# Optimization experiments

Measured on AMD Instinct MI355X. Metric: run time of the kernel, lower is better.

The kernel has to match this reference:

```python
import jax, jax.numpy as jnp
import numpy as np

# Static config (matches init_kwargs)
THR = 0.2
BORDER = 2
TEMP = 0.1
H0C, W0C = 60, 80
H1C, W1C = 60, 80
HW0_I = (480, 640)
SCALE = HW0_I[0] / H0C  # = 8.0, coarse->image scale


def setup_inputs() -> dict:
    key = jax.random.key(0)
    k0, k1 = jax.random.split(key)
    feat0 = jax.random.normal(k0, (4, H0C * W0C, 256), dtype=jnp.float32)
    feat1 = jax.random.normal(k1, (4, H1C * W1C, 256), dtype=jnp.float32)
    return {"feat0": feat0, "feat1": feat1}


def _valid_axis(n):
    i = jnp.arange(n)
    return (i >= BORDER) & (i < n - BORDER)


def reference(feat0, feat1):
    B, L, C = feat0.shape
    S = feat1.shape[1]
    inv_sqrt_c = 1.0 / jnp.sqrt(jnp.asarray(C, feat0.dtype))
    f0 = feat0 * inv_sqrt_c
    f1 = feat1 * inv_sqrt_c
    # similarity + dual softmax -> confidence matrix [B, L, S]
    sim = jnp.einsum("blc,bsc->bls", f0, f1) / TEMP
    conf = jax.nn.softmax(sim, axis=1) * jax.nn.softmax(sim, axis=2)

    # threshold + border removal (static border, no padding masks)
    mask = conf > THR
    m5 = mask.reshape(B, H0C, W0C, H1C, W1C)
    m5 = (m5
          & _valid_axis(H0C)[None, :, None, None, None]
          & _valid_axis(W0C)[None, None, :, None, None]
          & _valid_axis(H1C)[None, None, None, :, None]
          & _valid_axis(W1C)[None, None, None, None, :])
    mask = m5.reshape(B, L, S)

    # mutual nearest: keep conf only where it is both the row max and the col max
    score = mask.astype(conf.dtype) * jnp.max(conf, axis=2, keepdims=True) * jnp.max(conf, axis=1, keepdims=True)
    mask_max_values = jnp.max(score, axis=2)          # [B, L]
    s_ids = jnp.argmax(score, axis=2)                 # [B, L]
    match = mask_max_values > 0                       # [B, L] dense stand-in for torch.where
    mconf = jnp.take_along_axis(conf, s_ids[:, :, None], axis=2)[..., 0]
    mconf = jnp.where(match, mconf, jnp.zeros_like(mconf))

    # coarse keypoint coordinates
    l = jnp.arange(L)
    mkpts0 = jnp.stack([l % W0C, l // W0C], axis=1).astype(conf.dtype) * SCALE          # [L, 2]
    mkpts1 = jnp.stack([s_ids % W1C, s_ids // W1C], axis=-1).astype(conf.dtype) * SCALE  # [B, L, 2]
    return conf, match, s_ids, mconf, mkpts0, mkpts1
```

## Files before the change

kernel.cpp:

```cpp
#include <hip/hip_runtime.h>
#include <math.h>

#define B_ 4
#define L_ 4800
#define S_ 4800
#define C_ 256
#define LP_ 4864
#define THR 0.2f
#define SIM_SCALE 0.0390625f
#define KPT_SCALE 8.0f
#define CAND_CAP 262144u

typedef short bf16x8 __attribute__((ext_vector_type(8)));
typedef float f32x4  __attribute__((ext_vector_type(4)));

#define WS_ZERO_N 115204
#define WS_CAND_CNT 115200
#define WS_CAND_LIST 115208
#define WS_BF16 (115208 + CAND_CAP)

__device__ __forceinline__ unsigned short f2bf(float x) {
    union { float f; unsigned int u; } v; v.f = x;
    unsigned int r = v.u + 0x7fffu + ((v.u >> 16) & 1u);
    return (unsigned short)(r >> 16);
}

__device__ __forceinline__ void gload_lds16(const ushort* g, ushort* l) {
    __builtin_amdgcn_global_load_lds(
        (const __attribute__((address_space(1))) unsigned int*)g,
        (__attribute__((address_space(3))) unsigned int*)l,
        16, 0, 0);
}

__global__ void k_cast(const float* __restrict__ f0, const float* __restrict__ f1,
                       ushort* __restrict__ f0b, ushort* __restrict__ f1b,
                       float* __restrict__ ws) {
    const int i = blockIdx.x * blockDim.x + threadIdx.x;
    if (i < WS_ZERO_N) ws[i] = 0.0f;
    if (i * 4 >= B_ * L_ * C_) return;
    const int perb = L_ * C_ / 4;
    const int b    = i / perb;
    const int rem  = i - b * perb;
    float4 a = ((const float4*)f0)[i];
    float4 v = ((const float4*)f1)[i];
    ushort4 oa, ob;
    oa.x = f2bf(a.x); oa.y = f2bf(a.y); oa.z = f2bf(a.z); oa.w = f2bf(a.w);
    ob.x = f2bf(v.x); ob.y = f2bf(v.y); ob.z = f2bf(v.z); ob.w = f2bf(v.w);
    const int o = b * (LP_ * C_ / 4) + rem;
    ((ushort4*)f0b)[o] = oa;
    ((ushort4*)f1b)[o] = ob;
}

template <int PASS>
__global__ __launch_bounds__(256) void k_gemm(
        const ushort* __restrict__ f0b, const ushort* __restrict__ f1b,
        float* __restrict__ conf,
        float* __restrict__ rowsum, float* __restrict__ colsum,
        float* __restrict__ rowmax, float* __restrict__ colmax,
        unsigned* __restrict__ cand_cnt, unsigned* __restrict__ cand_list) {
    const int b    = blockIdx.z;
    const int l0   = blockIdx.y * 128;
    const int n0   = blockIdx.x * 128;
    const int t    = threadIdx.x;
    const int lane = t & 63;
    const int wid  = t >> 6;
    const int quad = lane >> 4;
    const int lr   = lane & 15;
    const int wr   = wid >> 1, wc = wid & 1;
    const int lw0  = l0 + wr * 64;
    const int nw0  = n0 + wc * 64;

    __shared__ ushort lA[128 * 32];
    __shared__ ushort lB[128 * 32];

    const ushort* A  = f0b + (size_t)b * LP_ * C_;
    const ushort* Bm = f1b + (size_t)b * LP_ * C_;

    f32x4 acc[4][4];
#pragma unroll
    for (int r = 0; r < 4; r++)
#pragma unroll
        for (int c = 0; c < 4; c++) acc[r][c] = (f32x4){0.f, 0.f, 0.f, 0.f};

    for (int kk = 0; kk < C_; kk += 32) {
#pragma unroll
        for (int i = 0; i < 2; i++) {
            const int e   = i * 256 + t;
            const int row = e >> 2;
            const int ch  = e & 3;
            gload_lds16(A  + (size_t)(l0 + row) * C_ + kk + ch * 8, &lA[e * 8]);
            gload_lds16(Bm + (size_t)(n0 + row) * C_ + kk + ch * 8, &lB[e * 8]);
        }
        __syncthreads();
        bf16x8 af[4], bf[4];
#pragma unroll
        for (int r = 0; r < 4; r++)
            af[r] = *(const bf16x8*)&lA[(wr * 64 + r * 16 + lr) * 32 + quad * 8];
#pragma unroll
        for (int c = 0; c < 4; c++)
            bf[c] = *(const bf16x8*)&lB[(wc * 64 + c * 16 + lr) * 32 + quad * 8];
#pragma unroll
        for (int r = 0; r < 4; r++)
#pragma unroll
            for (int c = 0; c < 4; c++)
                acc[r][c] = __builtin_amdgcn_mfma_f32_16x16x32_bf16(af[r], bf[c], acc[r][c], 0, 0, 0);
        __syncthreads();
    }

#pragma unroll
    for (int r = 0; r < 4; r++)
#pragma unroll
        for (int c = 0; c < 4; c++)
#pragma unroll
            for (int g = 0; g < 4; g++)
                acc[r][c][g] = __expf(acc[r][c][g] * SIM_SCALE);

    const bool edge = (lw0 + 63 >= L_) || (nw0 + 63 >= S_);
    if (edge) {
#pragma unroll
        for (int r = 0; r < 4; r++)
#pragma unroll
            for (int c = 0; c < 4; c++)
#pragma unroll
                for (int g = 0; g < 4; g++) {
                    const int l = lw0 + r * 16 + quad * 4 + g;
                    const int s = nw0 + c * 16 + lr;
                    if (l >= L_ || s >= S_) acc[r][c][g] = 0.f;
                }
    }

    if constexpr (PASS == 0) {
#pragma unroll
        for (int r = 0; r < 4; r++)
#pragma unroll
            for (int g = 0; g < 4; g++) {
                float v = acc[r][0][g] + acc[r][1][g] + acc[r][2][g] + acc[r][3][g];
                v += __shfl_xor(v, 1, 64);
                v += __shfl_xor(v, 2, 64);
                v += __shfl_xor(v, 4, 64);
                v += __shfl_xor(v, 8, 64);
                const int row = lw0 + r * 16 + quad * 4 + g;
                if (lr == 0 && row < L_) atomicAdd(rowsum + b * L_ + row, v);
            }
#pragma unroll
        for (int c = 0; c < 4; c++) {
            float v = 0.f;
#pragma unroll
            for (int r = 0; r < 4; r++)
#pragma unroll
                for (int g = 0; g < 4; g++) v += acc[r][c][g];
            v += __shfl_xor(v, 16, 64);
            v += __shfl_xor(v, 32, 64);
            const int s = nw0 + c * 16 + lr;
            if (quad == 0 && s < S_) atomicAdd(colsum + b * S_ + s, v);
        }
    } else {
        float irs[4][4];
#pragma unroll
        for (int r = 0; r < 4; r++)
#pragma unroll
            for (int g = 0; g < 4; g++) {
                const int l = lw0 + r * 16 + quad * 4 + g;
                irs[r][g] = 1.0f / rowsum[b * L_ + (l < L_ ? l : L_ - 1)];
            }
        float ics[4];
#pragma unroll
        for (int c = 0; c < 4; c++) {
            const int s = nw0 + c * 16 + lr;
            ics[c] = 1.0f / colsum[b * S_ + (s < S_ ? s : S_ - 1)];
        }
#pragma unroll
        for (int r = 0; r < 4; r++)
#pragma unroll
            for (int c = 0; c < 4; c++)
#pragma unroll
                for (int g = 0; g < 4; g++) {
                    const float p = acc[r][c][g];
                    acc[r][c][g] = p * p * (irs[r][g] * ics[c]);
                }

        float* pb = conf + (size_t)b * L_ * S_;
        if (!edge) {
#pragma unroll
            for (int r = 0; r < 4; r++)
#pragma unroll
                for (int g = 0; g < 4; g++) {
                    const int row = lw0 + r * 16 + quad * 4 + g;
                    float* prow = pb + (size_t)row * S_ + nw0 + lr;
#pragma unroll
                    for (int c = 0; c < 4; c++) prow[c * 16] = acc[r][c][g];
                }
        } else {
#pragma unroll
            for (int r = 0; r < 4; r++)
#pragma unroll
                for (int g = 0; g < 4; g++) {
                    const int row = lw0 + r * 16 + quad * 4 + g;
                    if (row < L_) {
                        float* prow = pb + (size_t)row * S_ + nw0 + lr;
#pragma unroll
                        for (int c = 0; c < 4; c++)
                            if (nw0 + c * 16 + lr < S_) prow[c * 16] = acc[r][c][g];
                    }
                }
        }

        float lane_max = 0.f;
#pragma unroll
        for (int r = 0; r < 4; r++)
#pragma unroll
            for (int g = 0; g < 4; g++) {
                float m = fmaxf(fmaxf(acc[r][0][g], acc[r][1][g]),
                                fmaxf(acc[r][2][g], acc[r][3][g]));
                lane_max = fmaxf(lane_max, m);
                m = fmaxf(m, __shfl_xor(m, 1, 64));
                m = fmaxf(m, __shfl_xor(m, 2, 64));
                m = fmaxf(m, __shfl_xor(m, 4, 64));
                m = fmaxf(m, __shfl_xor(m, 8, 64));
                const int row = lw0 + r * 16 + quad * 4 + g;
                if (lr == 0 && row < L_)
                    atomicMax((unsigned*)rowmax + b * L_ + row, __float_as_uint(m));
            }
#pragma unroll
        for (int c = 0; c < 4; c++) {
            float v = 0.f;
#pragma unroll
            for (int r = 0; r < 4; r++)
#pragma unroll
                for (int g = 0; g < 4; g++) v = fmaxf(v, acc[r][c][g]);
            v = fmaxf(v, __shfl_xor(v, 16, 64));
            v = fmaxf(v, __shfl_xor(v, 32, 64));
            const int s = nw0 + c * 16 + lr;
            if (quad == 0 && s < S_)
                atomicMax((unsigned*)colmax + b * S_ + s, __float_as_uint(v));
        }

        if (__any(lane_max > THR)) {
#pragma unroll
            for (int r = 0; r < 4; r++)
#pragma unroll
                for (int c = 0; c < 4; c++)
#pragma unroll
                    for (int g = 0; g < 4; g++) {
                        const float v = acc[r][c][g];
                        if (v > THR) {
                            const int l = lw0 + r * 16 + quad * 4 + g;
                            const int s = nw0 + c * 16 + lr;
                            const int lh = l / 80, lw = l % 80;
                            const int sh = s / 80, sw = s % 80;
                            if (lh >= 2 && lh < 58 && lw >= 2 && lw < 78 &&
                                sh >= 2 && sh < 58 && sw >= 2 && sw < 78) {
                                unsigned idx = atomicAdd(cand_cnt, 1u);
                                if (idx < CAND_CAP)
                                    cand_list[idx] = ((unsigned)b << 26) |
                                                     ((unsigned)l << 13) | (unsigned)s;
                            }
                        }
                    }
        }
    }
}

__global__ void k_score(const unsigned* __restrict__ cand_cnt,
                        const unsigned* __restrict__ cand_list,
                        const float* __restrict__ rowmax,
                        const float* __restrict__ colmax,
                        unsigned long long* __restrict__ best) {
    const unsigned n = min(*cand_cnt, CAND_CAP);
    for (unsigned i = blockIdx.x * blockDim.x + threadIdx.x; i < n;
         i += gridDim.x * blockDim.x) {
        const unsigned pk = cand_list[i];
        const int b = pk >> 26;
        const int l = (pk >> 13) & 8191;
        const int s = pk & 8191;
        const float sc = rowmax[b * L_ + l] * colmax[b * S_ + s];
        const unsigned long long key =
            ((unsigned long long)__float_as_uint(sc) << 32) |
            (unsigned long long)(0xFFFFFFFFu - (unsigned)s);
        atomicMax(best + b * L_ + l, key);
    }
}

__global__ void k_emit(const float* __restrict__ conf,
                       const unsigned long long* __restrict__ best,
                       float* __restrict__ o_match, float* __restrict__ o_sids,
                       float* __restrict__ o_mconf, float* __restrict__ o_kp0,
                       float* __restrict__ o_kp1) {
    const int i = blockIdx.x * blockDim.x + threadIdx.x;
    if (i >= B_ * L_) return;
    const int b = i / L_;
    const int l = i - b * L_;
    const unsigned long long key = best[i];
    const bool match = key != 0ull;
    const int sid = match ? (int)(0xFFFFFFFFu - (unsigned)(key & 0xFFFFFFFFull)) : 0;
    const float mc = match ? conf[(size_t)i * S_ + sid] : 0.0f;
    o_match[i] = match ? 1.0f : 0.0f;
    o_sids[i]  = (float)sid;
    o_mconf[i] = mc;
    o_kp1[i * 2 + 0] = (float)(sid % 80) * KPT_SCALE;
    o_kp1[i * 2 + 1] = (float)(sid / 80) * KPT_SCALE;
    if (b == 0) {
        o_kp0[l * 2 + 0] = (float)(l % 80) * KPT_SCALE;
        o_kp0[l * 2 + 1] = (float)(l / 80) * KPT_SCALE;
    }
}

extern "C" void kernel_launch(void* const* d_in, const int* in_sizes, int n_in,
                              void* d_out, int out_size, void* d_ws, size_t ws_size,
                              hipStream_t stream) {
    const float* f0 = (const float*)d_in[0];
    const float* f1 = (const float*)d_in[1];
    float* out = (float*)d_out;

    float* conf_o  = out;
    float* o_match = out + (size_t)92160000;
    float* o_sids  = o_match + 19200;
    float* o_mconf = o_sids + 19200;
    float* o_kp0   = o_mconf + 19200;
    float* o_kp1   = o_kp0 + 9600;

    float* wsf    = (float*)d_ws;
    float* rowsum = wsf;
    float* colsum = wsf + 19200;
    float* rowmax = wsf + 38400;
    float* colmax = wsf + 57600;
    unsigned long long* best = (unsigned long long*)(wsf + 76800);
    unsigned* cand_cnt  = (unsigned*)(wsf + WS_CAND_CNT);
    unsigned* cand_list = (unsigned*)(wsf + WS_CAND_LIST);
    ushort* f0b = (ushort*)(wsf + WS_BF16);
    ushort* f1b = f0b + (size_t)B_ * LP_ * C_;

    k_cast<<<4800, 256, 0, stream>>>(f0, f1, f0b, f1b, wsf);
    k_gemm<0><<<dim3(38, 38, B_), 256, 0, stream>>>(
        f0b, f1b, conf_o, rowsum, colsum, rowmax, colmax, cand_cnt, cand_list);
    k_gemm<1><<<dim3(38, 38, B_), 256, 0, stream>>>(
        f0b, f1b, conf_o, rowsum, colsum, rowmax, colmax, cand_cnt, cand_list);
    k_score<<<64, 256, 0, stream>>>(cand_cnt, cand_list, rowmax, colmax, best);
    k_emit<<<75, 256, 0, stream>>>(conf_o, best, o_match, o_sids, o_mconf, o_kp0, o_kp1);
}
```

Before: 646.0 us.

## Replace second GEMM pass with streaming normalization kernel over stored exp values

The GEMM now runs once, writing exp(sim) into the conf buffer while accumulating row and column sums. A new bandwidth-bound kernel rereads conf, applies the dual-softmax normalisation, writes it back, and computes row/col maxima plus threshold candidates using shared-memory reductions. This removes the recomputation of the full similarity GEMM. In exchange it adds an extra full read and write of the large conf tensor.

```diff
diff --git a/kernel.cpp b/kernel.cpp
--- a/kernel.cpp
+++ b/kernel.cpp
@@ -51,13 +51,10 @@
     ((ushort4*)f1b)[o] = ob;
 }
 
-template <int PASS>
 __global__ __launch_bounds__(256) void k_gemm(
         const ushort* __restrict__ f0b, const ushort* __restrict__ f1b,
         float* __restrict__ conf,
-        float* __restrict__ rowsum, float* __restrict__ colsum,
-        float* __restrict__ rowmax, float* __restrict__ colmax,
-        unsigned* __restrict__ cand_cnt, unsigned* __restrict__ cand_list) {
+        float* __restrict__ rowsum, float* __restrict__ colsum) {
     const int b    = blockIdx.z;
     const int l0   = blockIdx.y * 128;
     const int n0   = blockIdx.x * 128;
@@ -129,135 +126,121 @@
                 }
     }
 
-    if constexpr (PASS == 0) {
+    float* pb = conf + (size_t)b * L_ * S_;
+    if (!edge) {
 #pragma unroll
         for (int r = 0; r < 4; r++)
 #pragma unroll
             for (int g = 0; g < 4; g++) {
-                float v = acc[r][0][g] + acc[r][1][g] + acc[r][2][g] + acc[r][3][g];
-                v += __shfl_xor(v, 1, 64);
-                v += __shfl_xor(v, 2, 64);
-                v += __shfl_xor(v, 4, 64);
-                v += __shfl_xor(v, 8, 64);
                 const int row = lw0 + r * 16 + quad * 4 + g;
-                if (lr == 0 && row < L_) atomicAdd(rowsum + b * L_ + row, v);
+                float* prow = pb + (size_t)row * S_ + nw0 + lr;
+#pragma unroll
+                for (int c = 0; c < 4; c++) prow[c * 16] = acc[r][c][g];
             }
-#pragma unroll
-        for (int c = 0; c < 4; c++) {
-            float v = 0.f;
-#pragma unroll
-            for (int r = 0; r < 4; r++)
-#pragma unroll
-                for (int g = 0; g < 4; g++) v += acc[r][c][g];
-            v += __shfl_xor(v, 16, 64);
-            v += __shfl_xor(v, 32, 64);
-            const int s = nw0 + c * 16 + lr;
-            if (quad == 0 && s < S_) atomicAdd(colsum + b * S_ + s, v);
+    } else {
+#pragma unroll
+        for (int r = 0; r < 4; r++)
+#pragma unroll
+            for (int g = 0; g < 4; g++) {
+                const int row = lw0 + r * 16 + quad * 4 + g;
+                if (row < L_) {
+                    float* prow = pb + (size_t)row * S_ + nw0 + lr;
+#pragma unroll
+                    for (int c = 0; c < 4; c++)
+                        if (nw0 + c * 16 + lr < S_) prow[c * 16] = acc[r][c][g];
+                }
+            }
+    }
+
+#pragma unroll
+    for (int r = 0; r < 4; r++)
+#pragma unroll
+        for (int g = 0; g < 4; g++) {
+            float v = acc[r][0][g] + acc[r][1][g] + acc[r][2][g] + acc[r][3][g];
+            v += __shfl_xor(v, 1, 64);
+            v += __shfl_xor(v, 2, 64);
+            v += __shfl_xor(v, 4, 64);
+            v += __shfl_xor(v, 8, 64);
+            const int row = lw0 + r * 16 + quad * 4 + g;
+            if (lr == 0 && row < L_) atomicAdd(rowsum + b * L_ + row, v);
         }
-    } else {
-        float irs[4][4];
-#pragma unroll
-        for (int r = 0; r < 4; r++)
-#pragma unroll
-            for (int g = 0; g < 4; g++) {
-                const int l = lw0 + r * 16 + quad * 4 + g;
-                irs[r][g] = 1.0f / rowsum[b * L_ + (l < L_ ? l : L_ - 1)];
-            }
-        float ics[4];
-#pragma unroll
-        for (int c = 0; c < 4; c++) {
-            const int s = nw0 + c * 16 + lr;
-            ics[c] = 1.0f / colsum[b * S_ + (s < S_ ? s : S_ - 1)];
-        }
-#pragma unroll
-        for (int r = 0; r < 4; r++)
-#pragma unroll
-            for (int c = 0; c < 4; c++)
-#pragma unroll
-                for (int g = 0; g < 4; g++) {
-                    const float p = acc[r][c][g];
-                    acc[r][c][g] = p * p * (irs[r][g] * ics[c]);
-                }
-
-        float* pb = conf + (size_t)b * L_ * S_;
-        if (!edge) {
-#pragma unroll
-            for (int r = 0; r < 4; r++)
-#pragma unroll
-                for (int g = 0; g < 4; g++) {
-                    const int row = lw0 + r * 16 + quad * 4 + g;
-                    float* prow = pb + (size_t)row * S_ + nw0 + lr;
-#pragma unroll
-                    for (int c = 0; c < 4; c++) prow[c * 16] = acc[r][c][g];
-                }
-        } else {
-#pragma unroll
-            for (int r = 0; r < 4; r++)
-#pragma unroll
-                for (int g = 0; g < 4; g++) {
-                    const int row = lw0 + r * 16 + quad * 4 + g;
-                    if (row < L_) {
-                        float* prow = pb + (size_t)row * S_ + nw0 + lr;
-#pragma unroll
-                        for (int c = 0; c < 4; c++)
-                            if (nw0 + c * 16 + lr < S_) prow[c * 16] = acc[r][c][g];
+#pragma unroll
+    for (int c = 0; c < 4; c++) {
+        float v = 0.f;
+#pragma unroll
+        for (int r = 0; r < 4; r++)
+#pragma unroll
+            for (int g = 0; g < 4; g++) v += acc[r][c][g];
+        v += __shfl_xor(v, 16, 64);
+        v += __shfl_xor(v, 32, 64);
+        const int s = nw0 + c * 16 + lr;
+        if (quad == 0 && s < S_) atomicAdd(colsum + b * S_ + s, v);
+    }
+}
+
+__global__ __launch_bounds__(256) void k_norm(
+        float* __restrict__ conf,
+        const float* __restrict__ rowsum, const float* __restrict__ colsum,
+        float* __restrict__ rowmax, float* __restrict__ colmax,
+        unsigned* __restrict__ cand_cnt, unsigned* __restrict__ cand_list) {
+    const int b  = blockIdx.z;
+    const int l0 = blockIdx.y * 64;
+    const int s0 = blockIdx.x * 64;
+    __shared__ unsigned rm[64], cm[64];
+    const int t = threadIdx.x;
+    if (t < 64) { rm[t] = 0u; cm[t] = 0u; }
+    __syncthreads();
+    const int c4 = t & 15, r0 = t >> 4;
+    const int sbase = s0 + c4 * 4;
+    const float4 cs = *(const float4*)(colsum + b * S_ + sbase);
+    const float icx = 1.0f / cs.x, icy = 1.0f / cs.y, icz = 1.0f / cs.z, icw = 1.0f / cs.w;
+    float cmx = 0.f, cmy = 0.f, cmz = 0.f, cmw = 0.f;
+    float* base = conf + (size_t)b * L_ * S_;
+#pragma unroll
+    for (int it = 0; it < 4; it++) {
+        const int r = r0 + 16 * it;
+        const int l = l0 + r;
+        const float irs = 1.0f / rowsum[b * L_ + l];
+        float* addr = base + (size_t)l * S_ + sbase;
+        float4 p = *(float4*)addr;
+        float4 cf;
+        cf.x = p.x * p.x * (irs * icx);
+        cf.y = p.y * p.y * (irs * icy);
+        cf.z = p.z * p.z * (irs * icz);
+        cf.w = p.w * p.w * (irs * icw);
+        *(float4*)addr = cf;
+        const float m = fmaxf(fmaxf(cf.x, cf.y), fmaxf(cf.z, cf.w));
+        atomicMax(&rm[r], __float_as_uint(m));
+        cmx = fmaxf(cmx, cf.x); cmy = fmaxf(cmy, cf.y);
+        cmz = fmaxf(cmz, cf.z); cmw = fmaxf(cmw, cf.w);
+        if (m > THR) {
+            const int lh = l / 80, lw = l % 80;
+            if (lh >= 2 && lh < 58 && lw >= 2 && lw < 78) {
+                const float cfa[4] = {cf.x, cf.y, cf.z, cf.w};
+#pragma unroll
+                for (int j = 0; j < 4; j++) {
+                    if (cfa[j] > THR) {
+                        const int s = sbase + j;
+                        const int sh = s / 80, sw = s % 80;
+                        if (sh >= 2 && sh < 58 && sw >= 2 && sw < 78) {
+                            unsigned idx = atomicAdd(cand_cnt, 1u);
+                            if (idx < CAND_CAP)
+                                cand_list[idx] = ((unsigned)b << 26) |
+                                                 ((unsigned)l << 13) | (unsigned)s;
+                        }
                     }
                 }
+            }
         }
-
-        float lane_max = 0.f;
-#pragma unroll
-        for (int r = 0; r < 4; r++)
-#pragma unroll
-            for (int g = 0; g < 4; g++) {
-                float m = fmaxf(fmaxf(acc[r][0][g], acc[r][1][g]),
-                                fmaxf(acc[r][2][g], acc[r][3][g]));
-                lane_max = fmaxf(lane_max, m);
-                m = fmaxf(m, __shfl_xor(m, 1, 64));
-                m = fmaxf(m, __shfl_xor(m, 2, 64));
-                m = fmaxf(m, __shfl_xor(m, 4, 64));
-                m = fmaxf(m, __shfl_xor(m, 8, 64));
-                const int row = lw0 + r * 16 + quad * 4 + g;
-                if (lr == 0 && row < L_)
-                    atomicMax((unsigned*)rowmax + b * L_ + row, __float_as_uint(m));
-            }
-#pragma unroll
-        for (int c = 0; c < 4; c++) {
-            float v = 0.f;
-#pragma unroll
-            for (int r = 0; r < 4; r++)
-#pragma unroll
-                for (int g = 0; g < 4; g++) v = fmaxf(v, acc[r][c][g]);
-            v = fmaxf(v, __shfl_xor(v, 16, 64));
-            v = fmaxf(v, __shfl_xor(v, 32, 64));
-            const int s = nw0 + c * 16 + lr;
-            if (quad == 0 && s < S_)
-                atomicMax((unsigned*)colmax + b * S_ + s, __float_as_uint(v));
-        }
-
-        if (__any(lane_max > THR)) {
-#pragma unroll
-            for (int r = 0; r < 4; r++)
-#pragma unroll
-                for (int c = 0; c < 4; c++)
-#pragma unroll
-                    for (int g = 0; g < 4; g++) {
-                        const float v = acc[r][c][g];
-                        if (v > THR) {
-                            const int l = lw0 + r * 16 + quad * 4 + g;
-                            const int s = nw0 + c * 16 + lr;
-                            const int lh = l / 80, lw = l % 80;
-                            const int sh = s / 80, sw = s % 80;
-                            if (lh >= 2 && lh < 58 && lw >= 2 && lw < 78 &&
-                                sh >= 2 && sh < 58 && sw >= 2 && sw < 78) {
-                                unsigned idx = atomicAdd(cand_cnt, 1u);
-                                if (idx < CAND_CAP)
-                                    cand_list[idx] = ((unsigned)b << 26) |
-                                                     ((unsigned)l << 13) | (unsigned)s;
-                            }
-                        }
-                    }
-        }
+    }
+    atomicMax(&cm[c4 * 4 + 0], __float_as_uint(cmx));
+    atomicMax(&cm[c4 * 4 + 1], __float_as_uint(cmy));
+    atomicMax(&cm[c4 * 4 + 2], __float_as_uint(cmz));
+    atomicMax(&cm[c4 * 4 + 3], __float_as_uint(cmw));
+    __syncthreads();
+    if (t < 64) {
+        atomicMax((unsigned*)rowmax + b * L_ + l0 + t, rm[t]);
+        atomicMax((unsigned*)colmax + b * S_ + s0 + t, cm[t]);
     }
 }
 
@@ -331,10 +314,9 @@
     ushort* f1b = f0b + (size_t)B_ * LP_ * C_;
 
     k_cast<<<4800, 256, 0, stream>>>(f0, f1, f0b, f1b, wsf);
-    k_gemm<0><<<dim3(38, 38, B_), 256, 0, stream>>>(
-        f0b, f1b, conf_o, rowsum, colsum, rowmax, colmax, cand_cnt, cand_list);
-    k_gemm<1><<<dim3(38, 38, B_), 256, 0, stream>>>(
-        f0b, f1b, conf_o, rowsum, colsum, rowmax, colmax, cand_cnt, cand_list);
+    k_gemm<<<dim3(38, 38, B_), 256, 0, stream>>>(f0b, f1b, conf_o, rowsum, colsum);
+    k_norm<<<dim3(75, 75, B_), 256, 0, stream>>>(conf_o, rowsum, colsum,
+                                                 rowmax, colmax, cand_cnt, cand_list);
     k_score<<<64, 256, 0, stream>>>(cand_cnt, cand_list, rowmax, colmax, best);
     k_emit<<<75, 256, 0, stream>>>(conf_o, best, o_match, o_sids, o_mconf, o_kp0, o_kp1);
 }
```

Result: faster. 624.7 us (-3.3%).
